# Performance work log

Measured on AMD Instinct MI355X. Metric: run time of the kernel, lower is better.

## Reference

```python
import jax, jax.numpy as jnp
import numpy as np

N = 40000
E = 640000
IN_F, HID, OUT_F = 128, 128, 64


def setup_inputs() -> dict:
    key = jax.random.key(0)
    ks = jax.random.split(key, 6)
    x = jax.random.normal(ks[0], (N, IN_F), dtype=jnp.float32)
    edge_index = jax.random.randint(ks[1], (2, E), 0, N, dtype=jnp.int64)
    s_in = 1.0 / np.sqrt(IN_F)
    s_hid = 1.0 / np.sqrt(HID)
    W1l = jax.random.normal(ks[2], (IN_F, HID), dtype=jnp.float32) * s_in
    W1r = jax.random.normal(ks[3], (IN_F, HID), dtype=jnp.float32) * s_in
    b1 = jnp.zeros((HID,), dtype=jnp.float32)
    W2l = jax.random.normal(ks[4], (HID, OUT_F), dtype=jnp.float32) * s_hid
    W2r = jax.random.normal(ks[5], (HID, OUT_F), dtype=jnp.float32) * s_hid
    b2 = jnp.zeros((OUT_F,), dtype=jnp.float32)
    return {"x": x, "edge_index": edge_index, "W1l": W1l, "b1": b1,
            "W1r": W1r, "W2l": W2l, "b2": b2, "W2r": W2r}


def _mean_agg(x, src, dst, n_nodes):
    # mean of source-node features over incoming edges at each destination
    sums = jax.ops.segment_sum(x[src], dst, num_segments=n_nodes)  # [N, D]
    cnt = jax.ops.segment_sum(jnp.ones((src.shape[0],), x.dtype), dst,
                              num_segments=n_nodes)
    return sums / jnp.maximum(cnt, 1.0)[:, None]


def _sage_conv(x, src, dst, Wl, b, Wr, n_nodes):
    # PyG SAGEConv (mean aggr): lin_l(mean_j x_j) + lin_r(x_i), bias in lin_l
    agg = _mean_agg(x, src, dst, n_nodes)
    return agg @ Wl + b + x @ Wr


def reference(x, edge_index, W1l, b1, W1r, W2l, b2, W2r):
    src, dst = edge_index[0], edge_index[1]
    n = x.shape[0]
    h = jax.nn.relu(_sage_conv(x, src, dst, W1l, b1, W1r, n))
    return _sage_conv(h, src, dst, W2l, b2, W2r, n)
```

## Files before the change

### kernel.cpp

```cpp
#include <hip/hip_runtime.h>

#define NNODES 40000
#define NEDGES 640000
#define PAD 64

typedef unsigned int uint32;
typedef unsigned short ushort16;
typedef short bf16x8 __attribute__((ext_vector_type(8)));
typedef float f32x4 __attribute__((ext_vector_type(4)));

static __device__ __forceinline__ ushort16 f2bf(float f) {
    uint32 u = __builtin_bit_cast(uint32, f);
    uint32 r = u + 0x7fffu + ((u >> 16) & 1u);
    return (ushort16)(r >> 16);
}
static __device__ __forceinline__ float bf_lo(uint32 u) {
    uint32 t = u << 16;
    return __builtin_bit_cast(float, t);
}
static __device__ __forceinline__ float bf_hi(uint32 u) {
    uint32 t = u & 0xffff0000u;
    return __builtin_bit_cast(float, t);
}

static __device__ __forceinline__ void acc8(float* s, uint4 u) {
    s[0] += bf_lo(u.x); s[1] += bf_hi(u.x);
    s[2] += bf_lo(u.y); s[3] += bf_hi(u.y);
    s[4] += bf_lo(u.z); s[5] += bf_hi(u.z);
    s[6] += bf_lo(u.w); s[7] += bf_hi(u.w);
}

static __device__ __forceinline__ int edge_val(const void* ep, long long idx, int is64) {
    if (is64) return (int)((const long long*)ep)[idx];
    return ((const int*)ep)[idx];
}

__global__ void prep_kernel(const float* __restrict__ x, uint32* __restrict__ xbf2,
                            int* __restrict__ cnt,
                            const float* __restrict__ W1l, const float* __restrict__ W1r,
                            const float* __restrict__ W2l, const float* __restrict__ W2r,
                            ushort16* __restrict__ Wfrag1, ushort16* __restrict__ Wfrag2,
                            const int* __restrict__ e32, int* __restrict__ flag) {
    int b = blockIdx.x;
    if (b < 5000) {
        int i = b * 256 + threadIdx.x;
        if (i < NNODES) cnt[i] = 0;
        float4 v = ((const float4*)x)[i];
        uint2 o;
        o.x = (uint32)f2bf(v.x) | ((uint32)f2bf(v.y) << 16);
        o.y = (uint32)f2bf(v.z) | ((uint32)f2bf(v.w) << 16);
        ((uint2*)xbf2)[i] = o;
        return;
    }
    int i = (b - 5000) * 256 + threadIdx.x;
    if (i == 0) {
        int any = 0;
        for (int t = 0; t < 64; ++t) any |= e32[2 * t + 1];
        *flag = (any == 0) ? 1 : 0;
    }
    if (i < 32768) {
        int j = i & 7, lane = (i >> 3) & 63, nt = (i >> 9) & 7, s = (i >> 12) & 3, by = i >> 14;
        int k = s * 32 + (lane >> 4) * 8 + j;
        int col = nt * 16 + (lane & 15);
        float v = (by == 0) ? W1l[k * 128 + col] : W1r[k * 128 + col];
        Wfrag1[i] = f2bf(v);
    } else {
        int q = i - 32768;
        int j = q & 7, lane = (q >> 3) & 63, nt = (q >> 9) & 7, s = (q >> 12) & 3;
        int k = s * 32 + (lane >> 4) * 8 + j;
        int col = nt * 16 + (lane & 15);
        float v = (col < 64) ? W2l[k * 64 + col] : W2r[k * 64 + (col - 64)];
        Wfrag2[q] = f2bf(v);
    }
}

__global__ void build_kernel(const void* __restrict__ edges, const int* __restrict__ flag,
                             int* __restrict__ cnt, int* __restrict__ csr_src) {
    int e = blockIdx.x * 256 + threadIdx.x;
    if (e >= NEDGES) return;
    int is64 = *flag;
    int s = edge_val(edges, e, is64);
    int d = edge_val(edges, (long long)NEDGES + e, is64);
    int r = atomicAdd(&cnt[d], 1);
    if (r < PAD) csr_src[d * PAD + r] = s;
}

__global__ __launch_bounds__(256) void gemm_mfma_kernel(const ushort16* __restrict__ Abf,
                                                        const uint4* __restrict__ WfragG,
                                                        int Lw, int Rw,
                                                        ushort16* __restrict__ bfL,
                                                        ushort16* __restrict__ bfR,
                                                        float* __restrict__ fR) {
    __shared__ uint4 Bs[2048];
    int tid = threadIdx.x;
#pragma unroll
    for (int it = 0; it < 8; ++it) {
        int idx = tid + it * 256;
        Bs[idx] = WfragG[(size_t)blockIdx.y * 2048 + idx];
    }

    int wv = tid >> 6, lane = tid & 63;
    int quad = lane >> 4, c = lane & 15;
    int row0 = blockIdx.x * 64 + wv * 16;

    const uint4* arow = (const uint4*)(Abf + (size_t)(row0 + c) * 128);
    bf16x8 af[4];
#pragma unroll
    for (int s = 0; s < 4; ++s) af[s] = __builtin_bit_cast(bf16x8, arow[s * 4 + quad]);

    __syncthreads();

    f32x4 acc[8];
#pragma unroll
    for (int nt = 0; nt < 8; ++nt) acc[nt] = (f32x4){0.f, 0.f, 0.f, 0.f};

#pragma unroll
    for (int s = 0; s < 4; ++s) {
#pragma unroll
        for (int nt = 0; nt < 8; ++nt) {
            bf16x8 bf = __builtin_bit_cast(bf16x8, Bs[(s * 8 + nt) * 64 + lane]);
            acc[nt] = __builtin_amdgcn_mfma_f32_16x16x32_bf16(af[s], bf, acc[nt], 0, 0, 0);
        }
    }

    int colbase = blockIdx.y * 128;
#pragma unroll
    for (int nt = 0; nt < 8; ++nt) {
        int gcol = colbase + nt * 16 + c;
#pragma unroll
        for (int r = 0; r < 4; ++r) {
            int row = row0 + quad * 4 + r;
            if (gcol < Lw) {
                bfL[(size_t)row * Lw + gcol] = f2bf(acc[nt][r]);
            } else if (bfR) {
                bfR[(size_t)row * Rw + (gcol - Lw)] = f2bf(acc[nt][r]);
            } else {
                fR[(size_t)row * Rw + (gcol - Lw)] = acc[nt][r];
            }
        }
    }
}

__global__ __launch_bounds__(256) void agg1_kernel(const uint4* __restrict__ P4,
                                                   const uint4* __restrict__ S4,
                                                   const int* __restrict__ cnt,
                                                   const int* __restrict__ csr_src,
                                                   const float* __restrict__ b1,
                                                   uint4* __restrict__ hbf4) {
    int wave = threadIdx.x >> 6, lane = threadIdx.x & 63;
    int node = blockIdx.x * 4 + wave;
    if (node >= NNODES) return;
    int c = cnt[node];
    if (c > PAD) c = PAD;
    int beg = node * PAD;
    int sub = lane >> 4;
    int fl = lane & 15;
    float s[8];
#pragma unroll
    for (int i = 0; i < 8; ++i) s[i] = 0.f;

    int idx = 0;
    if (lane < c) idx = csr_src[beg + lane];
    int e = 0;
    for (; e + 8 <= c; e += 8) {
        int a0 = __shfl(idx, e + sub);
        int a1 = __shfl(idx, e + 4 + sub);
        uint4 u0 = P4[(size_t)a0 * 16 + fl];
        uint4 u1 = P4[(size_t)a1 * 16 + fl];
        acc8(s, u0);
        acc8(s, u1);
    }
    for (; e < c; e += 4) {
        int ee = e + sub;
        bool pred = ee < c;
        int a = __shfl(idx, pred ? ee : 0);
        uint4 u = P4[(size_t)a * 16 + fl];
        if (pred) acc8(s, u);
    }
#pragma unroll
    for (int i = 0; i < 8; ++i) s[i] += __shfl_xor(s[i], 16);
#pragma unroll
    for (int i = 0; i < 8; ++i) s[i] += __shfl_xor(s[i], 32);

    if (sub == 0) {
        float ic = 1.0f / (float)(c > 0 ? c : 1);
        uint4 su = S4[(size_t)node * 16 + fl];
        float4 bA = *(const float4*)&b1[fl * 8];
        float4 bB = *(const float4*)&b1[fl * 8 + 4];
        float sv[8];
        sv[0] = bf_lo(su.x); sv[1] = bf_hi(su.x);
        sv[2] = bf_lo(su.y); sv[3] = bf_hi(su.y);
        sv[4] = bf_lo(su.z); sv[5] = bf_hi(su.z);
        sv[6] = bf_lo(su.w); sv[7] = bf_hi(su.w);
        float bb[8] = {bA.x, bA.y, bA.z, bA.w, bB.x, bB.y, bB.z, bB.w};
        float v[8];
#pragma unroll
        for (int i = 0; i < 8; ++i) v[i] = fmaxf(fmaf(s[i], ic, bb[i] + sv[i]), 0.f);
        uint4 o;
        o.x = (uint32)f2bf(v[0]) | ((uint32)f2bf(v[1]) << 16);
        o.y = (uint32)f2bf(v[2]) | ((uint32)f2bf(v[3]) << 16);
        o.z = (uint32)f2bf(v[4]) | ((uint32)f2bf(v[5]) << 16);
        o.w = (uint32)f2bf(v[6]) | ((uint32)f2bf(v[7]) << 16);
        hbf4[(size_t)node * 16 + fl] = o;
    }
}

__global__ __launch_bounds__(256) void agg2_kernel(const uint4* __restrict__ P4,
                                                   const float* __restrict__ selfR2,
                                                   const int* __restrict__ cnt,
                                                   const int* __restrict__ csr_src,
                                                   const float* __restrict__ b2,
                                                   float* __restrict__ out) {
    int wave = threadIdx.x >> 6, lane = threadIdx.x & 63;
    int node = blockIdx.x * 4 + wave;
    if (node >= NNODES) return;
    int c = cnt[node];
    if (c > PAD) c = PAD;
    int beg = node * PAD;
    int sub = lane >> 3;
    int fl = lane & 7;
    float s[8];
#pragma unroll
    for (int i = 0; i < 8; ++i) s[i] = 0.f;

    int idx = 0;
    if (lane < c) idx = csr_src[beg + lane];
    int e = 0;
    for (; e + 16 <= c; e += 16) {
        int a0 = __shfl(idx, e + sub);
        int a1 = __shfl(idx, e + 8 + sub);
        uint4 u0 = P4[(size_t)a0 * 8 + fl];
        uint4 u1 = P4[(size_t)a1 * 8 + fl];
        acc8(s, u0);
        acc8(s, u1);
    }
    for (; e < c; e += 8) {
        int ee = e + sub;
        bool pred = ee < c;
        int a = __shfl(idx, pred ? ee : 0);
        uint4 u = P4[(size_t)a * 8 + fl];
        if (pred) acc8(s, u);
    }
#pragma unroll
    for (int i = 0; i < 8; ++i) s[i] += __shfl_xor(s[i], 8);
#pragma unroll
    for (int i = 0; i < 8; ++i) s[i] += __shfl_xor(s[i], 16);
#pragma unroll
    for (int i = 0; i < 8; ++i) s[i] += __shfl_xor(s[i], 32);

    if (sub == 0) {
        float ic = 1.0f / (float)(c > 0 ? c : 1);
        float4 sA = *(const float4*)&selfR2[(size_t)node * 64 + fl * 8];
        float4 sB = *(const float4*)&selfR2[(size_t)node * 64 + fl * 8 + 4];
        float4 bA = *(const float4*)&b2[fl * 8];
        float4 bB = *(const float4*)&b2[fl * 8 + 4];
        float sv[8] = {sA.x, sA.y, sA.z, sA.w, sB.x, sB.y, sB.z, sB.w};
        float bb[8] = {bA.x, bA.y, bA.z, bA.w, bB.x, bB.y, bB.z, bB.w};
        float v[8];
#pragma unroll
        for (int i = 0; i < 8; ++i) v[i] = fmaf(s[i], ic, bb[i] + sv[i]);
        float4 o0 = make_float4(v[0], v[1], v[2], v[3]);
        float4 o1 = make_float4(v[4], v[5], v[6], v[7]);
        *(float4*)&out[(size_t)node * 64 + fl * 8] = o0;
        *(float4*)&out[(size_t)node * 64 + fl * 8 + 4] = o1;
    }
}

extern "C" void kernel_launch(void* const* d_in, const int* in_sizes, int n_in,
                              void* d_out, int out_size, void* d_ws, size_t ws_size,
                              hipStream_t stream) {
    const float* x   = (const float*)d_in[0];
    const void*  ei  = d_in[1];
    const float* W1l = (const float*)d_in[2];
    const float* b1  = (const float*)d_in[3];
    const float* W1r = (const float*)d_in[4];
    const float* W2l = (const float*)d_in[5];
    const float* b2  = (const float*)d_in[6];
    const float* W2r = (const float*)d_in[7];
    float* out = (float*)d_out;

    char* p = (char*)d_ws;
    auto alloc = [&](size_t bytes) {
        char* r = p;
        p += (bytes + 255) & ~(size_t)255;
        return r;
    };
    int*      flag      = (int*)alloc(4);
    int*      cnt       = (int*)alloc(NNODES * 4);
    int*      csr_src   = (int*)alloc((size_t)NNODES * PAD * 4);
    ushort16* Wfrag1    = (ushort16*)alloc(32768 * 2);
    ushort16* Wfrag2    = (ushort16*)alloc(16384 * 2);
    uint32*   xbf       = (uint32*)alloc((size_t)NNODES * 64 * 4);
    ushort16* T1l       = (ushort16*)alloc((size_t)NNODES * 128 * 2);
    ushort16* T1r       = (ushort16*)alloc((size_t)NNODES * 128 * 2);
    uint32*   hbf       = (uint32*)alloc((size_t)NNODES * 64 * 4);
    ushort16* T2l       = (ushort16*)alloc((size_t)NNODES * 64 * 2);
    float*    T2r       = (float*)alloc((size_t)NNODES * 64 * 4);

    prep_kernel<<<5192, 256, 0, stream>>>(x, xbf, cnt, W1l, W1r, W2l, W2r, Wfrag1, Wfrag2,
                                          (const int*)ei, flag);
    build_kernel<<<(NEDGES + 255) / 256, 256, 0, stream>>>(ei, flag, cnt, csr_src);

    gemm_mfma_kernel<<<dim3(NNODES / 64, 2), 256, 0, stream>>>(
        (const ushort16*)xbf, (const uint4*)Wfrag1, 128, 128, T1l, T1r, (float*)nullptr);
    agg1_kernel<<<(NNODES + 3) / 4, 256, 0, stream>>>((const uint4*)T1l, (const uint4*)T1r,
                                                      cnt, csr_src, b1, (uint4*)hbf);

    gemm_mfma_kernel<<<dim3(NNODES / 64, 1), 256, 0, stream>>>(
        (const ushort16*)hbf, (const uint4*)Wfrag2, 64, 64, T2l, (ushort16*)nullptr, T2r);
    agg2_kernel<<<(NNODES + 3) / 4, 256, 0, stream>>>((const uint4*)T2l, T2r, cnt, csr_src, b2,
                                                      out);
}
```

Before: 184.9 us.

## Build CSR via two-pass bucketed binning with shared-memory atomics

```diff
diff --git a/kernel.cpp b/kernel.cpp
--- a/kernel.cpp
+++ b/kernel.cpp
@@ -3,6 +3,10 @@
 #define NNODES 40000
 #define NEDGES 640000
 #define PAD 64
+#define NBK 160
+#define BNODES 250
+#define BCAP 8192
+#define ACHUNK 4000
 
 typedef unsigned int uint32;
 typedef unsigned short ushort16;
@@ -36,7 +40,7 @@
 }
 
 __global__ void prep_kernel(const float* __restrict__ x, uint32* __restrict__ xbf2,
-                            int* __restrict__ cnt,
+                            int* __restrict__ gcur,
                             const float* __restrict__ W1l, const float* __restrict__ W1r,
                             const float* __restrict__ W2l, const float* __restrict__ W2r,
                             ushort16* __restrict__ Wfrag1, ushort16* __restrict__ Wfrag2,
@@ -44,7 +48,6 @@
     int b = blockIdx.x;
     if (b < 5000) {
         int i = b * 256 + threadIdx.x;
-        if (i < NNODES) cnt[i] = 0;
         float4 v = ((const float4*)x)[i];
         uint2 o;
         o.x = (uint32)f2bf(v.x) | ((uint32)f2bf(v.y) << 16);
@@ -53,6 +56,7 @@
         return;
     }
     int i = (b - 5000) * 256 + threadIdx.x;
+    if (i < NBK) gcur[i] = 0;
     if (i == 0) {
         int any = 0;
         for (int t = 0; t < 64; ++t) any |= e32[2 * t + 1];
@@ -74,15 +78,68 @@
     }
 }
 
-__global__ void build_kernel(const void* __restrict__ edges, const int* __restrict__ flag,
-                             int* __restrict__ cnt, int* __restrict__ csr_src) {
-    int e = blockIdx.x * 256 + threadIdx.x;
-    if (e >= NEDGES) return;
+__global__ __launch_bounds__(256) void buildA_kernel(const void* __restrict__ edges,
+                                                     const int* __restrict__ flag,
+                                                     int* __restrict__ gcur,
+                                                     int* __restrict__ bstream) {
+    __shared__ int hist[NBK];
+    __shared__ int cur[NBK];
+    int tid = threadIdx.x;
+    int base = blockIdx.x * ACHUNK;
+    for (int i = tid; i < NBK; i += 256) hist[i] = 0;
+    __syncthreads();
     int is64 = *flag;
-    int s = edge_val(edges, e, is64);
-    int d = edge_val(edges, (long long)NEDGES + e, is64);
-    int r = atomicAdd(&cnt[d], 1);
-    if (r < PAD) csr_src[d * PAD + r] = s;
+#pragma unroll
+    for (int k = 0; k < (ACHUNK + 255) / 256; ++k) {
+        int off = k * 256 + tid;
+        if (off < ACHUNK) {
+            int d = edge_val(edges, (long long)NEDGES + base + off, is64);
+            atomicAdd(&hist[d / BNODES], 1);
+        }
+    }
+    __syncthreads();
+    if (tid < NBK) cur[tid] = atomicAdd(&gcur[tid], hist[tid]);
+    __syncthreads();
+#pragma unroll
+    for (int k = 0; k < (ACHUNK + 255) / 256; ++k) {
+        int off = k * 256 + tid;
+        if (off < ACHUNK) {
+            int e = base + off;
+            int d = edge_val(edges, (long long)NEDGES + e, is64);
+            int s = edge_val(edges, e, is64);
+            int bk = d / BNODES;
+            int dloc = d - bk * BNODES;
+            int r = atomicAdd(&cur[bk], 1);
+            if (r < BCAP) bstream[bk * BCAP + r] = (s << 8) | dloc;
+        }
+    }
+}
+
+__global__ __launch_bounds__(256) void buildB_kernel(const int* __restrict__ bstream,
+                                                     const int* __restrict__ gcur,
+                                                     int* __restrict__ cnt,
+                                                     int* __restrict__ csr_src) {
+    __shared__ int4 img4[BNODES * 16];
+    __shared__ int hist[BNODES];
+    int* img = (int*)img4;
+    int tid = threadIdx.x;
+    int bk = blockIdx.x;
+    for (int i = tid; i < BNODES; i += 256) hist[i] = 0;
+    __syncthreads();
+    int n = gcur[bk];
+    if (n > BCAP) n = BCAP;
+    for (int i = tid; i < n; i += 256) {
+        int u = bstream[bk * BCAP + i];
+        int dloc = u & 255;
+        int s = u >> 8;
+        int r = atomicAdd(&hist[dloc], 1);
+        if (r < PAD) img[dloc * PAD + r] = s;
+    }
+    __syncthreads();
+    int4* csr4 = (int4*)csr_src;
+#pragma unroll
+    for (int i = tid; i < BNODES * 16; i += 256) csr4[(size_t)bk * BNODES * 16 + i] = img4[i];
+    for (int i = tid; i < BNODES; i += 256) cnt[bk * BNODES + i] = hist[i];
 }
 
 __global__ __launch_bounds__(256) void gemm_mfma_kernel(const ushort16* __restrict__ Abf,
@@ -287,6 +344,8 @@
     };
     int*      flag      = (int*)alloc(4);
     int*      cnt       = (int*)alloc(NNODES * 4);
+    int*      gcur      = (int*)alloc(NBK * 4);
+    int*      bstream   = (int*)alloc((size_t)NBK * BCAP * 4);
     int*      csr_src   = (int*)alloc((size_t)NNODES * PAD * 4);
     ushort16* Wfrag1    = (ushort16*)alloc(32768 * 2);
     ushort16* Wfrag2    = (ushort16*)alloc(16384 * 2);
@@ -297,9 +356,10 @@
     ushort16* T2l       = (ushort16*)alloc((size_t)NNODES * 64 * 2);
     float*    T2r       = (float*)alloc((size_t)NNODES * 64 * 4);
 
-    prep_kernel<<<5192, 256, 0, stream>>>(x, xbf, cnt, W1l, W1r, W2l, W2r, Wfrag1, Wfrag2,
+    prep_kernel<<<5192, 256, 0, stream>>>(x, xbf, gcur, W1l, W1r, W2l, W2r, Wfrag1, Wfrag2,
                                           (const int*)ei, flag);
-    build_kernel<<<(NEDGES + 255) / 256, 256, 0, stream>>>(ei, flag, cnt, csr_src);
+    buildA_kernel<<<NBK, 256, 0, stream>>>(ei, flag, gcur, bstream);
+    buildB_kernel<<<NBK, 256, 0, stream>>>(bstream, gcur, cnt, csr_src);
 
     gemm_mfma_kernel<<<dim3(NNODES / 64, 2), 256, 0, stream>>>(
         (const ushort16*)xbf, (const uint4*)Wfrag1, 128, 128, T1l, T1r, (float*)nullptr);
```

Result: faster. 175.6 us (-5.0%).
